# Kernel tuning notes

Hardware: AMD Instinct MI355X
Metric: run time of the kernel (lower is better)

## Reference

```python
import jax, jax.numpy as jnp
import numpy as np

V, E, H = 50257, 256, 256
B, S = 4, 1024
MAX_DEPTH, K = 2, 2
THR = 0.5
SIB_SCALE = 1.0 / np.sqrt(H)
EPS = 1e-8
P_MIN, P_MAX = 1e-7, 1.0 - 1e-7


def setup_inputs() -> dict:
    key = jax.random.key(0)
    ks = jax.random.split(key, 10)
    return {
        'tokens': jax.random.randint(ks[0], (B, S), 0, V),
        'embedding': 0.02 * jax.random.normal(ks[1], (V, E), jnp.float32),
        'proj_W': jax.random.normal(ks[2], (H, E), jnp.float32) / np.sqrt(E),
        'proj_b': jnp.zeros((H,), jnp.float32),
        'child_W': jax.random.normal(ks[3], (H, H), jnp.float32) / np.sqrt(H),
        'child_b': jnp.zeros((H,), jnp.float32),
        'sib_emb': 0.02 * jax.random.normal(ks[4], (K, H), jnp.float32),
        'depth_emb': 0.02 * jax.random.normal(ks[5], (MAX_DEPTH, H), jnp.float32),
        'pol_W1': jax.random.normal(ks[6], (H, H), jnp.float32) / np.sqrt(H),
        'pol_b1': jnp.zeros((H,), jnp.float32),
        'pol_w2': jax.random.normal(ks[7], (H,), jnp.float32) / np.sqrt(H),
        'pol_b2': jnp.zeros((), jnp.float32),
        'out_W': jax.random.normal(ks[8], (V, H), jnp.float32) / np.sqrt(H),
        'out_b': jnp.zeros((V,), jnp.float32),
    }


def reference(tokens, embedding, proj_W, proj_b, child_W, child_b, sib_emb,
              depth_emb, pol_W1, pol_b1, pol_w2, pol_b2, out_W, out_b):
    # Greedy (inference) BFS rollout, fully masked/vectorized over the fixed
    # max tree (1 + K + K^2 nodes per token position).
    b, s = tokens.shape
    h0 = jnp.take(embedding, tokens, axis=0) @ proj_W.T + proj_b  # [B,S,H]
    level_h = h0[:, :, None, :]                                    # [B,S,1,H]
    level_mask = jnp.ones(level_h.shape[:3], level_h.dtype)        # [B,S,1]
    sum_h = (level_h * level_mask[..., None]).sum(axis=2)          # [B,S,H]
    cnt = level_mask.sum(axis=2)                                   # [B,S]
    for d in range(MAX_DEPTH):
        # growth policy: sigmoid MLP conditioned on depth embedding
        z = jnp.tanh(level_h @ pol_W1.T + pol_b1 + depth_emb[d])   # [B,S,n,H]
        p = jax.nn.sigmoid(z @ pol_w2 + pol_b2)                    # [B,S,n]
        p = jnp.clip(p, P_MIN, P_MAX)  # _safe_clamp_prob
        grow = (p >= THR).astype(level_h.dtype) * level_mask       # greedy
        # child transform + scaled sibling position embedding
        base = jnp.tanh(level_h @ child_W.T + child_b)             # [B,S,n,H]
        child = base[:, :, :, None, :] + SIB_SCALE * sib_emb       # [B,S,n,K,H]
        child_mask = jnp.broadcast_to(grow[..., None], child.shape[:4])
        level_h = child.reshape(b, s, -1, H)
        level_mask = child_mask.reshape(b, s, -1)
        sum_h = sum_h + (level_h * level_mask[..., None]).sum(axis=2)
        cnt = cnt + level_mask.sum(axis=2)
    pooled = sum_h / (cnt[..., None] + EPS)                        # mean pooling
    logits = pooled @ out_W.T + out_b                              # [B,S,V]
    return logits
```

## Files before the change

kernel.cpp:

```cpp
#include <hip/hip_runtime.h>
#include <stdint.h>

#define VOCAB 50257
#define NP    50304
#define H     256
#define BS    4096
#define K3    256
#define SIB   0.0625f

typedef __attribute__((ext_vector_type(8))) _Float16 f16x8;
typedef __attribute__((ext_vector_type(4))) float f32x4;

__device__ __forceinline__ void gload_lds16(const void* g, void* l) {
  __builtin_amdgcn_global_load_lds(
      (const __attribute__((address_space(1))) void*)g,
      (__attribute__((address_space(3))) void*)l, 16, 0, 0);
}

__global__ __launch_bounds__(256) void k_tr(const float* __restrict__ pW,
                                            const float* __restrict__ qW,
                                            const float* __restrict__ cW,
                                            float* __restrict__ WT) {
  __shared__ float T[64][65];
  const int blk = blockIdx.x;
  const int m = blk >> 4, t = blk & 15;
  const float* src = (m == 0) ? pW : (m == 1) ? qW : cW;
  float* dst = WT + m * 65536;
  const int tr = (t >> 2) * 64, tc = (t & 3) * 64;
  const int r = threadIdx.x >> 6, c = threadIdx.x & 63;
#pragma unroll
  for (int i = 0; i < 16; ++i) {
    const int row = r * 16 + i;
    T[row][c] = src[(tr + row) * H + tc + c];
  }
  __syncthreads();
#pragma unroll
  for (int i = 0; i < 16; ++i) {
    const int row = r * 16 + i;
    dst[(tc + row) * H + tr + c] = T[c][row];
  }
}

__global__ __launch_bounds__(256) void k_sib(const float* __restrict__ WT,
                                             const float* __restrict__ sib_emb,
                                             float* __restrict__ sibproj) {
  const int b = blockIdx.x;
  const float* Wt = WT + ((b < 2) ? 65536 : 131072);
  const float* v = sib_emb + (b & 1) * H;
  const int h = threadIdx.x;
  float acc = 0.f;
  for (int e4 = 0; e4 < 64; ++e4) {
    const float4 s = *(const float4*)(v + e4 * 4);
    acc += Wt[(e4 * 4 + 0) * H + h] * s.x;
    acc += Wt[(e4 * 4 + 1) * H + h] * s.y;
    acc += Wt[(e4 * 4 + 2) * H + h] * s.z;
    acc += Wt[(e4 * 4 + 3) * H + h] * s.w;
  }
  sibproj[b * H + h] = acc;
}

__global__ __launch_bounds__(256) void k_conv(const float* __restrict__ W,
                                              _Float16* __restrict__ B2) {
  const int64_t nit = (int64_t)NP * 32;
  for (int64_t i = (int64_t)blockIdx.x * blockDim.x + threadIdx.x; i < nit;
       i += (int64_t)gridDim.x * blockDim.x) {
    const int v = (int)(i >> 5);
    const int h8 = ((int)i & 31) * 8;
    float4 w0, w1;
    if (v < VOCAB) {
      w0 = *(const float4*)(W + (int64_t)v * H + h8);
      w1 = *(const float4*)(W + (int64_t)v * H + h8 + 4);
    } else {
      w0 = make_float4(0.f, 0.f, 0.f, 0.f);
      w1 = w0;
    }
    _Float16 o[8] = {(_Float16)w0.x, (_Float16)w0.y, (_Float16)w0.z, (_Float16)w0.w,
                     (_Float16)w1.x, (_Float16)w1.y, (_Float16)w1.z, (_Float16)w1.w};
    *(f16x8*)(B2 + (int64_t)v * K3 + h8) = *(f16x8*)o;
  }
}

#define MATVEC_T(WTp, SRC, ACC)                                                   \
  do {                                                                            \
    _Pragma("unroll") for (int j = 0; j < 4; ++j)                                 \
        _Pragma("unroll") for (int tt = 0; tt < 4; ++tt) ACC[j][tt] = 0.f;        \
    _Pragma("unroll 2") for (int e4 = 0; e4 < 64; ++e4) {                         \
      float4 s4[4];                                                               \
      _Pragma("unroll") for (int tt = 0; tt < 4; ++tt)                            \
          s4[tt] = *(const float4*)&SRC[tg * 4 + tt][e4 * 4];                     \
      _Pragma("unroll") for (int u = 0; u < 4; ++u) {                             \
        const int e = e4 * 4 + u;                                                 \
        float wt[4];                                                              \
        _Pragma("unroll") for (int j = 0; j < 4; ++j)                             \
            wt[j] = (WTp)[e * H + hg + 64 * j];                                   \
        _Pragma("unroll") for (int j = 0; j < 4; ++j)                             \
            _Pragma("unroll") for (int tt = 0; tt < 4; ++tt)                      \
                ACC[j][tt] += wt[j] * ((const float*)&s4[tt])[u];                 \
      }                                                                           \
    }                                                                             \
  } while (0)

#define REDUCE_TO_X(slot)                                                \
  do {                                                                   \
    const int rt = tid >> 4, rl = tid & 15;                              \
    float part = 0.f;                                                    \
    _Pragma("unroll") for (int i = 0; i < 16; ++i) part +=               \
        ZW[rt][rl + 16 * i];                                             \
    part += __shfl_xor(part, 1, 16);                                     \
    part += __shfl_xor(part, 2, 16);                                     \
    part += __shfl_xor(part, 4, 16);                                     \
    part += __shfl_xor(part, 8, 16);                                     \
    if (rl == 0) X[slot][rt] = part + b2;                                \
  } while (0)

__global__ __launch_bounds__(256) void k_pooled(
    const int* __restrict__ tokens, const float* __restrict__ emb,
    const float* __restrict__ WT, const float* __restrict__ proj_b,
    const float* __restrict__ child_b,
    const float* __restrict__ sib_emb, const float* __restrict__ depth_emb,
    const float* __restrict__ pol_b1,
    const float* __restrict__ pol_w2, const float* __restrict__ pol_b2,
    const float* __restrict__ sibproj, _Float16* __restrict__ A2) {
  __shared__ float IN[16][256];
  __shared__ float H0[16][256];
  __shared__ float B0s[16][256];
  __shared__ float ZW[16][264];
  __shared__ float X[3][16];
  __shared__ int TOK[16];
  const int tid = threadIdx.x;
  const int hg = tid & 63;
  const int tg = tid >> 6;
  const int t0 = blockIdx.x * 16;
  const float b2 = pol_b2[0];
  const float* projT = WT;
  const float* polT = WT + 65536;
  const float* childT = WT + 131072;

  float sibs[4];
#pragma unroll
  for (int j = 0; j < 4; ++j) {
    const int hj = hg + 64 * j;
    sibs[j] = SIB * (sib_emb[hj] + sib_emb[H + hj]);
  }

  if (tid < 16) TOK[tid] = tokens[t0 + tid];
  __syncthreads();
  for (int t = 0; t < 16; ++t) IN[t][tid] = emb[(int64_t)TOK[t] * H + tid];
  __syncthreads();

  float acc[4][4], sum[4][4];

  MATVEC_T(projT, IN, acc);
#pragma unroll
  for (int j = 0; j < 4; ++j) {
    const int hj = hg + 64 * j;
    const float pb = proj_b[hj];
#pragma unroll
    for (int tt = 0; tt < 4; ++tt) {
      const float h0v = acc[j][tt] + pb;
      H0[tg * 4 + tt][hj] = h0v;
      sum[j][tt] = h0v;
    }
  }
  __syncthreads();

  MATVEC_T(polT, H0, acc);
#pragma unroll
  for (int j = 0; j < 4; ++j) {
    const int hj = hg + 64 * j;
    const float pb1 = pol_b1[hj], de0 = depth_emb[hj], w2 = pol_w2[hj];
#pragma unroll
    for (int tt = 0; tt < 4; ++tt) {
      const float z = tanhf(acc[j][tt] + pb1 + de0);
      ZW[tg * 4 + tt][hj] = z * w2;
    }
  }
  __syncthreads();
  REDUCE_TO_X(0);
  __syncthreads();

  MATVEC_T(childT, H0, acc);
#pragma unroll
  for (int j = 0; j < 4; ++j) {
    const int hj = hg + 64 * j;
    const float cb = child_b[hj];
#pragma unroll
    for (int tt = 0; tt < 4; ++tt) {
      const float base0 = tanhf(acc[j][tt] + cb);
      B0s[tg * 4 + tt][hj] = base0;
      const float g0 = (X[0][tg * 4 + tt] >= 0.f) ? 1.f : 0.f;
      sum[j][tt] += g0 * (2.f * base0 + sibs[j]);
    }
  }
  __syncthreads();

  float accP[4][4];
  MATVEC_T(polT, B0s, accP);
#pragma unroll
  for (int k = 0; k < 2; ++k) {
#pragma unroll
    for (int j = 0; j < 4; ++j) {
      const int hj = hg + 64 * j;
      const float pb1 = pol_b1[hj], de1 = depth_emb[H + hj], w2 = pol_w2[hj];
      const float ps = sibproj[k * H + hj];
#pragma unroll
      for (int tt = 0; tt < 4; ++tt) {
        const float z = tanhf(accP[j][tt] + SIB * ps + pb1 + de1);
        ZW[tg * 4 + tt][hj] = z * w2;
      }
    }
    __syncthreads();
    if (k == 0) REDUCE_TO_X(1); else REDUCE_TO_X(2);
    __syncthreads();
  }

  MATVEC_T(childT, B0s, acc);
#pragma unroll
  for (int j = 0; j < 4; ++j) {
    const int hj = hg + 64 * j;
    const float cb = child_b[hj];
    const float cs0 = sibproj[2 * H + hj], cs1 = sibproj[3 * H + hj];
#pragma unroll
    for (int tt = 0; tt < 4; ++tt) {
      const int t = tg * 4 + tt;
      const float g0 = (X[0][t] >= 0.f) ? 1.f : 0.f;
      const float m0 = (g0 > 0.f && X[1][t] >= 0.f) ? 1.f : 0.f;
      const float m1 = (g0 > 0.f && X[2][t] >= 0.f) ? 1.f : 0.f;
      const float bk0 = tanhf(acc[j][tt] + SIB * cs0 + cb);
      const float bk1 = tanhf(acc[j][tt] + SIB * cs1 + cb);
      float s = sum[j][tt] + m0 * (2.f * bk0 + sibs[j]) + m1 * (2.f * bk1 + sibs[j]);
      const float cnt = 1.f + 2.f * g0 + 2.f * (m0 + m1);
      const float pooled = s / (cnt + 1e-8f);
      A2[(int64_t)(t0 + t) * K3 + hj] = (_Float16)pooled;
    }
  }
}

__global__ __launch_bounds__(256) void k_gemm(const _Float16* __restrict__ A2,
                                              const _Float16* __restrict__ B2,
                                              const float* __restrict__ out_b,
                                              float* __restrict__ C) {
  __shared__ __align__(16) char smem[65536];
  const int tid = threadIdx.x;
  const int lane = tid & 63;
  const int w = tid >> 6;
  const int wg = blockIdx.x;
  const int xcd = wg & 7;
  const int local = wg >> 3;
  const int m_l = local / 393;
  const int n_l = local - m_l * 393;
  const int m0 = (xcd * 4 + m_l) * 128;
  const int n0 = n_l * 128;
  f32x4 acc[4][4] = {};

  const int rl = lane >> 3;
  const int gsw = (lane & 7) ^ rl;
  const _Float16* gA = A2 + (int64_t)(m0 + w * 32 + rl) * K3 + gsw * 8;
  const _Float16* gB = B2 + (int64_t)(n0 + w * 32 + rl) * K3 + gsw * 8;

  const int fr = lane & 15;
  const int g = lane >> 4;
  const int am = (w >> 1) * 64;
  const int bn = (w & 1) * 64;

#define LBAR()                                                   \
  do {                                                           \
    __builtin_amdgcn_sched_barrier(0);                           \
    asm volatile("s_waitcnt lgkmcnt(0)" ::: "memory");           \
    __builtin_amdgcn_s_barrier();                                \
    __builtin_amdgcn_sched_barrier(0);                           \
  } while (0)

#define STAGE(c, t)                                                          \
  do {                                                                       \
    _Pragma("unroll") for (int q = 0; q < 4; ++q) {                          \
      gload_lds16(gA + (int64_t)q * 8 * K3 + (t) * 64,                       \
                  (_Float16*)(smem + (c) * 32768) + (w * 32 + q * 8) * 64);  \
      gload_lds16(gB + (int64_t)q * 8 * K3 + (t) * 64,                       \
                  (_Float16*)(smem + (c) * 32768 + 16384) +                  \
                      (w * 32 + q * 8) * 64);                                \
    }                                                                        \
  } while (0)

  STAGE(0, 0);

  for (int t = 0; t < 4; ++t) {
    const int cur = t & 1;
    if (t < 3) {
      STAGE(cur ^ 1, t + 1);
      asm volatile("s_waitcnt vmcnt(8)" ::: "memory");
    } else {
      asm volatile("s_waitcnt vmcnt(0)" ::: "memory");
    }
    __builtin_amdgcn_s_barrier();
    __builtin_amdgcn_sched_barrier(0);
    const _Float16* At = (const _Float16*)(smem + cur * 32768);
    const _Float16* Bt = (const _Float16*)(smem + cur * 32768 + 16384);
#pragma unroll
    for (int kk = 0; kk < 2; ++kk) {
      f16x8 af[4], bf[4];
#pragma unroll
      for (int i = 0; i < 4; ++i)
        af[i] = *(const f16x8*)(At + (am + i * 16 + fr) * 64 +
                                (((kk * 4 + g) ^ (fr & 7)) * 8));
#pragma unroll
      for (int i = 0; i < 4; ++i)
        bf[i] = *(const f16x8*)(Bt + (bn + i * 16 + fr) * 64 +
                                (((kk * 4 + g) ^ (fr & 7)) * 8));
#pragma unroll
      for (int i = 0; i < 4; ++i)
#pragma unroll
        for (int j = 0; j < 4; ++j)
          acc[i][j] = __builtin_amdgcn_mfma_f32_16x16x32_f16(af[i], bf[j], acc[i][j], 0, 0, 0);
    }
    __builtin_amdgcn_sched_barrier(0);
    __builtin_amdgcn_s_barrier();
  }

  float biasj[4];
#pragma unroll
  for (int j = 0; j < 4; ++j) {
    const int gn = n0 + bn + j * 16 + fr;
    biasj[j] = (gn < VOCAB) ? out_b[gn] : 0.f;
  }
  float* L = (float*)smem;
#pragma unroll
  for (int q = 0; q < 4; ++q) {
#pragma unroll
    for (int j = 0; j < 4; ++j) {
      const int lcol = bn + j * 16 + fr;
#pragma unroll
      for (int r = 0; r < 4; ++r) {
        const int lrow = (w >> 1) * 16 + g * 4 + r;
        L[lrow * 132 + lcol] = acc[q][j][r] + biasj[j];
      }
    }
    LBAR();
#pragma unroll
    for (int pass = 0; pass < 4; ++pass) {
      const int lr = pass * 8 + (tid >> 5);
      const int colq = (tid & 31) * 4;
      const int gm = m0 + (lr >> 4) * 64 + q * 16 + (lr & 15);
      const int gcol = n0 + colq;
      const f32x4 v = *(const f32x4*)&L[lr * 132 + colq];
      float* cp = C + (int64_t)gm * VOCAB + gcol;
      if (gcol + 4 <= VOCAB) {
        __builtin_nontemporal_store(v, (f32x4*)cp);
      } else {
#pragma unroll
        for (int e = 0; e < 4; ++e)
          if (gcol + e < VOCAB) __builtin_nontemporal_store(v[e], cp + e);
      }
    }
    LBAR();
  }
#undef STAGE
#undef LBAR
}

extern "C" void kernel_launch(void* const* d_in, const int* in_sizes, int n_in,
                              void* d_out, int out_size, void* d_ws, size_t ws_size,
                              hipStream_t stream) {
  const int* tokens = (const int*)d_in[0];
  const float* embedding = (const float*)d_in[1];
  const float* proj_W = (const float*)d_in[2];
  const float* proj_b = (const float*)d_in[3];
  const float* child_W = (const float*)d_in[4];
  const float* child_b = (const float*)d_in[5];
  const float* sib_emb = (const float*)d_in[6];
  const float* depth_emb = (const float*)d_in[7];
  const float* pol_W1 = (const float*)d_in[8];
  const float* pol_b1 = (const float*)d_in[9];
  const float* pol_w2 = (const float*)d_in[10];
  const float* pol_b2 = (const float*)d_in[11];
  const float* out_W = (const float*)d_in[12];
  const float* out_b = (const float*)d_in[13];
  float* C = (float*)d_out;
  char* ws = (char*)d_ws;
  _Float16* B2 = (_Float16*)ws;
  _Float16* A2 = (_Float16*)(ws + 25755648);
  float* sibproj = (float*)(ws + 27852800);
  float* WT = (float*)(ws + 27856896);

  k_tr<<<48, 256, 0, stream>>>(proj_W, pol_W1, child_W, WT);
  k_sib<<<4, 256, 0, stream>>>(WT, sib_emb, sibproj);
  k_conv<<<2048, 256, 0, stream>>>(out_W, B2);
  k_pooled<<<256, 256, 0, stream>>>(tokens, embedding, WT, proj_b, child_b,
                                    sib_emb, depth_emb, pol_b1,
                                    pol_w2, pol_b2, sibproj, A2);
  k_gemm<<<12576, 256, 0, stream>>>(A2, B2, out_b, C);
}
```

Measured before the change: 406.9 us.

## Enlarge GEMM tiles to 256x256 with 512-thread blocks and K-step 32

New measurement: 466.6 us. +14.7%, slower.

```diff
diff --git a/kernel.cpp b/kernel.cpp
--- a/kernel.cpp
+++ b/kernel.cpp
@@ -2,7 +2,7 @@
 #include <stdint.h>
 
 #define VOCAB 50257
-#define NP    50304
+#define NP2   50432
 #define H     256
 #define BS    4096
 #define K3    256
@@ -61,7 +61,7 @@
 
 __global__ __launch_bounds__(256) void k_conv(const float* __restrict__ W,
                                               _Float16* __restrict__ B2) {
-  const int64_t nit = (int64_t)NP * 32;
+  const int64_t nit = (int64_t)NP2 * 32;
   for (int64_t i = (int64_t)blockIdx.x * blockDim.x + threadIdx.x; i < nit;
        i += (int64_t)gridDim.x * blockDim.x) {
     const int v = (int)(i >> 5);
@@ -236,32 +236,29 @@
   }
 }
 
-__global__ __launch_bounds__(256) void k_gemm(const _Float16* __restrict__ A2,
-                                              const _Float16* __restrict__ B2,
-                                              const float* __restrict__ out_b,
-                                              float* __restrict__ C) {
+__global__ __launch_bounds__(512, 2) void k_gemm(const _Float16* __restrict__ A2,
+                                                 const _Float16* __restrict__ B2,
+                                                 const float* __restrict__ out_b,
+                                                 float* __restrict__ C) {
   __shared__ __align__(16) char smem[65536];
   const int tid = threadIdx.x;
   const int lane = tid & 63;
   const int w = tid >> 6;
+  const int wr = w >> 2;
+  const int wc = w & 3;
   const int wg = blockIdx.x;
   const int xcd = wg & 7;
   const int local = wg >> 3;
-  const int m_l = local / 393;
-  const int n_l = local - m_l * 393;
-  const int m0 = (xcd * 4 + m_l) * 128;
-  const int n0 = n_l * 128;
-  f32x4 acc[4][4] = {};
-
-  const int rl = lane >> 3;
-  const int gsw = (lane & 7) ^ rl;
-  const _Float16* gA = A2 + (int64_t)(m0 + w * 32 + rl) * K3 + gsw * 8;
-  const _Float16* gB = B2 + (int64_t)(n0 + w * 32 + rl) * K3 + gsw * 8;
-
+  const int m_l = local / 197;
+  const int n_l = local - m_l * 197;
+  const int m0 = (xcd * 2 + m_l) * 256;
+  const int n0 = n_l * 256;
+  f32x4 acc[8][4] = {};
+
+  const int srow = lane >> 2;
+  const int gsw = (lane & 3) ^ (srow & 3);
   const int fr = lane & 15;
   const int g = lane >> 4;
-  const int am = (w >> 1) * 64;
-  const int bn = (w & 1) * 64;
 
 #define LBAR()                                                   \
   do {                                                           \
@@ -271,24 +268,26 @@
     __builtin_amdgcn_sched_barrier(0);                           \
   } while (0)
 
-#define STAGE(c, t)                                                          \
-  do {                                                                       \
-    _Pragma("unroll") for (int q = 0; q < 4; ++q) {                          \
-      gload_lds16(gA + (int64_t)q * 8 * K3 + (t) * 64,                       \
-                  (_Float16*)(smem + (c) * 32768) + (w * 32 + q * 8) * 64);  \
-      gload_lds16(gB + (int64_t)q * 8 * K3 + (t) * 64,                       \
-                  (_Float16*)(smem + (c) * 32768 + 16384) +                  \
-                      (w * 32 + q * 8) * 64);                                \
-    }                                                                        \
+#define STAGE(c, t)                                                           \
+  do {                                                                        \
+    _Pragma("unroll") for (int q = 0; q < 2; ++q) {                           \
+      gload_lds16(A2 + (int64_t)(m0 + w * 32 + q * 16 + srow) * K3 +          \
+                      (t) * 32 + gsw * 8,                                     \
+                  (_Float16*)(smem + (c) * 32768) + (w * 32 + q * 16) * 32);  \
+      gload_lds16(B2 + (int64_t)(n0 + w * 32 + q * 16 + srow) * K3 +          \
+                      (t) * 32 + gsw * 8,                                     \
+                  (_Float16*)(smem + (c) * 32768 + 16384) +                   \
+                      (w * 32 + q * 16) * 32);                                \
+    }                                                                         \
   } while (0)
 
   STAGE(0, 0);
 
-  for (int t = 0; t < 4; ++t) {
+  for (int t = 0; t < 8; ++t) {
     const int cur = t & 1;
-    if (t < 3) {
+    if (t < 7) {
       STAGE(cur ^ 1, t + 1);
-      asm volatile("s_waitcnt vmcnt(8)" ::: "memory");
+      asm volatile("s_waitcnt vmcnt(4)" ::: "memory");
     } else {
       asm volatile("s_waitcnt vmcnt(0)" ::: "memory");
     }
@@ -296,54 +295,49 @@
     __builtin_amdgcn_sched_barrier(0);
     const _Float16* At = (const _Float16*)(smem + cur * 32768);
     const _Float16* Bt = (const _Float16*)(smem + cur * 32768 + 16384);
-#pragma unroll
-    for (int kk = 0; kk < 2; ++kk) {
-      f16x8 af[4], bf[4];
-#pragma unroll
-      for (int i = 0; i < 4; ++i)
-        af[i] = *(const f16x8*)(At + (am + i * 16 + fr) * 64 +
-                                (((kk * 4 + g) ^ (fr & 7)) * 8));
-#pragma unroll
-      for (int i = 0; i < 4; ++i)
-        bf[i] = *(const f16x8*)(Bt + (bn + i * 16 + fr) * 64 +
-                                (((kk * 4 + g) ^ (fr & 7)) * 8));
-#pragma unroll
-      for (int i = 0; i < 4; ++i)
-#pragma unroll
-        for (int j = 0; j < 4; ++j)
-          acc[i][j] = __builtin_amdgcn_mfma_f32_16x16x32_f16(af[i], bf[j], acc[i][j], 0, 0, 0);
-    }
+    f16x8 af[8], bf[4];
+#pragma unroll
+    for (int mi = 0; mi < 8; ++mi)
+      af[mi] = *(const f16x8*)(At + (wr * 128 + mi * 16 + fr) * 32 +
+                               ((g ^ (fr & 3)) * 8));
+#pragma unroll
+    for (int ni = 0; ni < 4; ++ni)
+      bf[ni] = *(const f16x8*)(Bt + (wc * 64 + ni * 16 + fr) * 32 +
+                               ((g ^ (fr & 3)) * 8));
+#pragma unroll
+    for (int mi = 0; mi < 8; ++mi)
+#pragma unroll
+      for (int ni = 0; ni < 4; ++ni)
+        acc[mi][ni] = __builtin_amdgcn_mfma_f32_16x16x32_f16(af[mi], bf[ni], acc[mi][ni], 0, 0, 0);
     __builtin_amdgcn_sched_barrier(0);
     __builtin_amdgcn_s_barrier();
   }
 
-  float biasj[4];
-#pragma unroll
-  for (int j = 0; j < 4; ++j) {
-    const int gn = n0 + bn + j * 16 + fr;
-    biasj[j] = (gn < VOCAB) ? out_b[gn] : 0.f;
+  float biasn[4];
+#pragma unroll
+  for (int ni = 0; ni < 4; ++ni) {
+    const int gn = n0 + wc * 64 + ni * 16 + fr;
+    biasn[ni] = (gn < VOCAB) ? out_b[gn] : 0.f;
   }
   float* L = (float*)smem;
 #pragma unroll
-  for (int q = 0; q < 4; ++q) {
-#pragma unroll
-    for (int j = 0; j < 4; ++j) {
-      const int lcol = bn + j * 16 + fr;
-#pragma unroll
-      for (int r = 0; r < 4; ++r) {
-        const int lrow = (w >> 1) * 16 + g * 4 + r;
-        L[lrow * 132 + lcol] = acc[q][j][r] + biasj[j];
-      }
+  for (int mi = 0; mi < 8; ++mi) {
+#pragma unroll
+    for (int ni = 0; ni < 4; ++ni) {
+      const int lcol = wc * 64 + ni * 16 + fr;
+#pragma unroll
+      for (int r = 0; r < 4; ++r)
+        L[(wr * 16 + g * 4 + r) * 260 + lcol] = acc[mi][ni][r] + biasn[ni];
     }
     LBAR();
 #pragma unroll
     for (int pass = 0; pass < 4; ++pass) {
-      const int lr = pass * 8 + (tid >> 5);
-      const int colq = (tid & 31) * 4;
-      const int gm = m0 + (lr >> 4) * 64 + q * 16 + (lr & 15);
-      const int gcol = n0 + colq;
-      const f32x4 v = *(const f32x4*)&L[lr * 132 + colq];
-      float* cp = C + (int64_t)gm * VOCAB + gcol;
+      const int lr = tid >> 4;
+      const int col = (tid & 15) * 4 + pass * 64;
+      const int gr = m0 + (lr >> 4) * 128 + mi * 16 + (lr & 15);
+      const int gcol = n0 + col;
+      const f32x4 v = *(const f32x4*)&L[lr * 260 + col];
+      float* cp = C + (int64_t)gr * VOCAB + gcol;
       if (gcol + 4 <= VOCAB) {
         __builtin_nontemporal_store(v, (f32x4*)cp);
       } else {
@@ -378,9 +372,9 @@
   float* C = (float*)d_out;
   char* ws = (char*)d_ws;
   _Float16* B2 = (_Float16*)ws;
-  _Float16* A2 = (_Float16*)(ws + 25755648);
-  float* sibproj = (float*)(ws + 27852800);
-  float* WT = (float*)(ws + 27856896);
+  _Float16* A2 = (_Float16*)(ws + 25821184);
+  float* sibproj = (float*)(ws + 27918336);
+  float* WT = (float*)(ws + 27922432);
 
   k_tr<<<48, 256, 0, stream>>>(proj_W, pol_W1, child_W, WT);
   k_sib<<<4, 256, 0, stream>>>(WT, sib_emb, sibproj);
@@ -388,5 +382,5 @@
   k_pooled<<<256, 256, 0, stream>>>(tokens, embedding, WT, proj_b, child_b,
                                     sib_emb, depth_emb, pol_b1,
                                     pol_w2, pol_b2, sibproj, A2);
-  k_gemm<<<12576, 256, 0, stream>>>(A2, B2, out_b, C);
-}
+  k_gemm<<<3152, 512, 0, stream>>>(A2, B2, out_b, C);
+}
```
